# Kernel tuning notes

Hardware: AMD Instinct MI355X
Metric: run time of the kernel (lower is better)

The kernel has to match this reference:

```python
import jax, jax.numpy as jnp
import numpy as np

B, S, H = 1, 2048, 4096
NQ, NKV, D = 32, 8, 128
N_REP = NQ // NKV
SCALE = 1.0 / np.sqrt(D)
SOFTCAP = 30.0
EPS = 1e-5


def _rotate_half(x):
    x1, x2 = jnp.split(x, 2, axis=-1)
    return jnp.concatenate([-x2, x1], axis=-1)


def _rms_norm(x, w, eps=EPS):
    xf = x.astype(jnp.float32)
    norm = xf * jax.lax.rsqrt(jnp.mean(xf * xf, axis=-1, keepdims=True) + eps)
    return (w * norm).astype(x.dtype)


def setup_inputs() -> dict:
    key = jax.random.key(0)
    ks = jax.random.split(key, 8)
    hidden_states = jax.random.normal(ks[0], (B, S, H), dtype=jnp.float32)
    # causal additive mask
    causal = jnp.tril(jnp.ones((S, S), dtype=bool))
    attention_mask = jnp.where(causal, 0.0, -1e9)[None, None].astype(jnp.float32)
    # RoPE cache
    inv_freq = 1.0 / (10000.0 ** (np.arange(0, D, 2, dtype=np.float32) / D))
    t = np.arange(S, dtype=np.float32)
    freqs = np.outer(t, inv_freq)                      # (S, D/2)
    emb = np.concatenate([freqs, freqs], axis=-1)      # (S, D)
    cos = jnp.asarray(np.cos(emb))[None, None]         # (1,1,S,D)
    sin = jnp.asarray(np.sin(emb))[None, None]
    # params
    std = 0.02
    wq = jax.random.normal(ks[1], (NQ * D, H), dtype=jnp.float32) * std
    wk = jax.random.normal(ks[2], (NKV * D, H), dtype=jnp.float32) * std
    wv = jax.random.normal(ks[3], (NKV * D, H), dtype=jnp.float32) * std
    wo = jax.random.normal(ks[4], (H, NQ * D), dtype=jnp.float32) * std
    pre_norm_w = jnp.ones((H,), dtype=jnp.float32)
    q_norm_w = jnp.ones((D,), dtype=jnp.float32)
    k_norm_w = jnp.ones((D,), dtype=jnp.float32)
    return {
        "hidden_states": hidden_states, "attention_mask": attention_mask,
        "cos": cos, "sin": sin, "pre_norm_w": pre_norm_w,
        "wq": wq, "wk": wk, "wv": wv, "wo": wo,
        "q_norm_w": q_norm_w, "k_norm_w": k_norm_w,
    }


def reference(hidden_states, attention_mask, cos, sin, pre_norm_w,
              wq, wk, wv, wo, q_norm_w, k_norm_w):
    residual = hidden_states
    h = _rms_norm(hidden_states, pre_norm_w)
    bsz, seq_len, _ = h.shape
    # projections -> (b, heads, s, d)
    q = jnp.einsum('bsh,eh->bse', h, wq).reshape(bsz, seq_len, NQ, D).transpose(0, 2, 1, 3)
    k = jnp.einsum('bsh,eh->bse', h, wk).reshape(bsz, seq_len, NKV, D).transpose(0, 2, 1, 3)
    v = jnp.einsum('bsh,eh->bse', h, wv).reshape(bsz, seq_len, NKV, D).transpose(0, 2, 1, 3)
    # QK RMSNorm over head_dim
    q = _rms_norm(q, q_norm_w)
    k = _rms_norm(k, k_norm_w)
    # RoPE (full head_dim)
    q = q * cos + _rotate_half(q) * sin
    k = k * cos + _rotate_half(k) * sin
    # GQA: repeat kv heads
    k_exp = jnp.repeat(k, N_REP, axis=1)  # (b, NQ, s, d)
    v_exp = jnp.repeat(v, N_REP, axis=1)
    scores = jnp.einsum('bhqd,bhkd->bhqk', q, k_exp) * SCALE
    scores = SOFTCAP * jnp.tanh(scores / SOFTCAP)
    scores = scores + attention_mask
    probs = jax.nn.softmax(scores.astype(jnp.float32), axis=-1).astype(q.dtype)
    attn = jnp.einsum('bhqk,bhkd->bhqd', probs, v_exp)
    attn = attn.transpose(0, 2, 1, 3).reshape(bsz, seq_len, NQ * D)
    out = jnp.einsum('bse,he->bsh', attn, wo)
    return residual + out
```

## Files before the change

### kernel.cpp

```cpp
#include <hip/hip_runtime.h>
#include <cstdint>

typedef __bf16 bf16;
typedef __bf16 bf16x8 __attribute__((ext_vector_type(8)));
typedef __bf16 bf16x4 __attribute__((ext_vector_type(4)));
typedef float  f32x4  __attribute__((ext_vector_type(4)));

#define SEQ  2048
#define HID  4096
#define DH   128
#define NQH  32
#define NKVH 8
#define NTOT 6144
#define RSCALE 0.08838834764831845f
#define SOFTCAP 30.0f
#define L2E 1.4426950408889634f

__device__ __forceinline__ void gl2lds16(const void* g, void* l) {
  __builtin_amdgcn_global_load_lds(
      (const __attribute__((address_space(1))) unsigned int*)g,
      (__attribute__((address_space(3))) unsigned int*)l, 16, 0, 0);
}

__global__ void cvt_kernel(const float* __restrict__ in, bf16* __restrict__ out, int n4) {
  const int stride = gridDim.x * blockDim.x;
  for (int i = blockIdx.x * blockDim.x + threadIdx.x; i < n4; i += stride) {
    const float4 v = ((const float4*)in)[i];
    bf16x4 o = { (bf16)v.x, (bf16)v.y, (bf16)v.z, (bf16)v.w };
    *(bf16x4*)(out + (size_t)i * 4) = o;
  }
}

__global__ void rmsnorm_kernel(const float* __restrict__ x, const float* __restrict__ w,
                               bf16* __restrict__ out) {
  const int s = blockIdx.x;
  const float* xr = x + (size_t)s * HID;
  float4 v[4];
  float ss = 0.f;
#pragma unroll
  for (int j = 0; j < 4; ++j) {
    v[j] = ((const float4*)xr)[threadIdx.x + j * 256];
    ss += v[j].x * v[j].x + v[j].y * v[j].y + v[j].z * v[j].z + v[j].w * v[j].w;
  }
#pragma unroll
  for (int m = 1; m < 64; m <<= 1) ss += __shfl_xor(ss, m);
  __shared__ float red[4];
  if ((threadIdx.x & 63) == 0) red[threadIdx.x >> 6] = ss;
  __syncthreads();
  const float rn = rsqrtf((red[0] + red[1] + red[2] + red[3]) * (1.f / HID) + 1e-5f);
  bf16* orow = out + (size_t)s * HID;
#pragma unroll
  for (int j = 0; j < 4; ++j) {
    const int idx = (threadIdx.x + j * 256) * 4;
    const float4 wv = ((const float4*)w)[threadIdx.x + j * 256];
    bf16x4 o = { (bf16)(v[j].x * rn * wv.x), (bf16)(v[j].y * rn * wv.y),
                 (bf16)(v[j].z * rn * wv.z), (bf16)(v[j].w * rn * wv.w) };
    *(bf16x4*)(orow + idx) = o;
  }
}

template<bool FINAL>
__global__ __launch_bounds__(512, 2)
void gemm256(const bf16* __restrict__ A, const bf16* __restrict__ B,
             bf16* __restrict__ Cb, float* __restrict__ Cf,
             const float* __restrict__ resid, int M, int N, int K)
{
  extern __shared__ char smem[];
  const int tid  = threadIdx.x;
  const int lane = tid & 63;
  const int wave = tid >> 6;
  const int wm = wave >> 2, wn = wave & 3;

  const int gx = gridDim.x;
  const int nwg = gx * gridDim.y;
  int lin = blockIdx.x + gx * blockIdx.y;
  lin = (lin & 7) * (nwg >> 3) + (lin >> 3);
  const int m0 = (lin / gx) * 256;
  const int n0 = (lin % gx) * 256;

  auto Abuf = [&](int b) -> bf16* { return (bf16*)(smem + b * 65536); };
  auto Bbuf = [&](int b) -> bf16* { return (bf16*)(smem + b * 65536 + 32768); };

  auto stage = [&](int kt, int b) {
    bf16* Ad = Abuf(b);
    bf16* Bd = Bbuf(b);
#pragma unroll
    for (int i = 0; i < 4; ++i) {
      const int c = i * 8 + wave;
      const int row = c * 8 + (lane >> 3);
      const int col8 = (lane & 7) ^ (row & 7);
      gl2lds16(A + (size_t)(m0 + row) * K + kt + col8 * 8, Ad + c * 512);
    }
#pragma unroll
    for (int i = 0; i < 4; ++i) {
      const int c = i * 8 + wave;
      const int row = c * 8 + (lane >> 3);
      const int col8 = (lane & 7) ^ (row & 7);
      gl2lds16(B + (size_t)(n0 + row) * K + kt + col8 * 8, Bd + c * 512);
    }
  };

  f32x4 acc[8][4] = {};
  const int nt = K / 64;

  stage(0, 0);
  asm volatile("s_waitcnt vmcnt(0)" ::: "memory");
  __builtin_amdgcn_s_barrier();

  for (int t = 0; t < nt; ++t) {
    const int p = t & 1;
    const bf16* Ab = Abuf(p);
    const bf16* Bb = Bbuf(p);
    bf16x8 bfr[4][2];

#pragma unroll
    for (int q = 0; q < 4; ++q) {
      bf16x8 afr[2][2];
#pragma unroll
      for (int mi = 0; mi < 2; ++mi)
#pragma unroll
        for (int ks = 0; ks < 2; ++ks) {
          const int row = wm * 128 + q * 32 + mi * 16 + (lane & 15);
          const int slot = (ks * 4 + (lane >> 4)) ^ (row & 7);
          afr[mi][ks] = *(const bf16x8*)(Ab + row * 64 + slot * 8);
        }
      if (q == 0) {
#pragma unroll
        for (int ni = 0; ni < 4; ++ni)
#pragma unroll
          for (int ks = 0; ks < 2; ++ks) {
            const int row = wn * 64 + ni * 16 + (lane & 15);
            const int slot = (ks * 4 + (lane >> 4)) ^ (row & 7);
            bfr[ni][ks] = *(const bf16x8*)(Bb + row * 64 + slot * 8);
          }
        if (t + 1 < nt) stage((t + 1) * 64, p ^ 1);
      }

      __builtin_amdgcn_s_barrier();
      asm volatile("s_waitcnt lgkmcnt(0)" ::: "memory");
      __builtin_amdgcn_sched_barrier(0);
      __builtin_amdgcn_s_setprio(1);
#pragma unroll
      for (int ks = 0; ks < 2; ++ks)
#pragma unroll
        for (int mi = 0; mi < 2; ++mi)
#pragma unroll
          for (int ni = 0; ni < 4; ++ni)
            acc[q * 2 + mi][ni] = __builtin_amdgcn_mfma_f32_16x16x32_bf16(
                afr[mi][ks], bfr[ni][ks], acc[q * 2 + mi][ni], 0, 0, 0);
      __builtin_amdgcn_s_setprio(0);

      if (q == 3 && t + 1 < nt)
        asm volatile("s_waitcnt vmcnt(0)" ::: "memory");
      __builtin_amdgcn_s_barrier();
    }
  }

#pragma unroll
  for (int a = 0; a < 8; ++a) {
#pragma unroll
    for (int i = 0; i < 4; ++i) {
      const int m = m0 + wm * 128 + (a >> 1) * 32 + (a & 1) * 16 + (lane >> 4) * 4 + i;
#pragma unroll
      for (int ni = 0; ni < 4; ++ni) {
        const int n = n0 + wn * 64 + ni * 16 + (lane & 15);
        const float v = acc[a][ni][i];
        if constexpr (FINAL) {
          Cf[(size_t)m * N + n] = v + resid[(size_t)m * N + n];
        } else {
          Cb[(size_t)m * N + n] = (bf16)v;
        }
      }
    }
  }
}

__global__ void qkrope_kernel(const bf16* __restrict__ qkv,
                              const float* __restrict__ qw, const float* __restrict__ kw,
                              const float* __restrict__ cs, const float* __restrict__ sn,
                              bf16* __restrict__ qr, bf16* __restrict__ kr)
{
  const int w = blockIdx.x * 4 + (threadIdx.x >> 6);
  const int lane = threadIdx.x & 63;
  const int s = w / (NQH + NKVH);
  const int hh = w % (NQH + NKVH);
  const bf16* src; bf16* dst; const float* nw;
  if (hh < NQH) {
    src = qkv + (size_t)s * NTOT + hh * DH;
    dst = qr + ((size_t)hh * SEQ + s) * DH;
    nw = qw;
  } else {
    const int h2 = hh - NQH;
    src = qkv + (size_t)s * NTOT + 4096 + h2 * DH;
    dst = kr + ((size_t)h2 * SEQ + s) * DH;
    nw = kw;
  }
  const float x0 = (float)src[lane], x1 = (float)src[lane + 64];
  float ss = x0 * x0 + x1 * x1;
#pragma unroll
  for (int m = 1; m < 64; m <<= 1) ss += __shfl_xor(ss, m);
  const float rn = rsqrtf(ss * (1.f / DH) + 1e-5f);
  const float n0 = x0 * rn * nw[lane], n1 = x1 * rn * nw[lane + 64];
  const float c0 = cs[s * DH + lane],      s0 = sn[s * DH + lane];
  const float c1 = cs[s * DH + lane + 64], s1 = sn[s * DH + lane + 64];
  dst[lane]      = (bf16)(n0 * c0 - n1 * s0);
  dst[lane + 64] = (bf16)(n1 * c1 + n0 * s1);
}

__global__ void vtrans_kernel(const bf16* __restrict__ qkv, bf16* __restrict__ vt)
{
  __shared__ bf16 tbuf[64][33];
  const int s0 = blockIdx.x * 64;
  const int d0 = blockIdx.y * 32;
  const int h  = blockIdx.z;
  const int tid = threadIdx.x;
  {
    const int col = tid & 31, r0 = tid >> 5;
    for (int r = r0; r < 64; r += 8)
      tbuf[r][col] = qkv[(size_t)(s0 + r) * NTOT + 5120 + h * DH + d0 + col];
  }
  __syncthreads();
  {
    const int sc = tid & 63, dr0 = tid >> 6;
    for (int d = dr0; d < 32; d += 4)
      vt[((size_t)h * DH + d0 + d) * SEQ + s0 + sc] = tbuf[sc][d];
  }
}

__global__ __launch_bounds__(256, 2)
void attn_kernel(const bf16* __restrict__ Q, const bf16* __restrict__ Kr,
                 const bf16* __restrict__ Vt, bf16* __restrict__ Oa)
{
  __shared__ bf16 Ks[2][64 * 128];
  __shared__ bf16 Vs[2][128 * 64];
  __shared__ bf16 Ps[4][32 * 64];

  const int tid = threadIdx.x, lane = tid & 63, wave = tid >> 6;

  const int lin  = blockIdx.x + 16 * blockIdx.y;
  const int slot = lin >> 8, idx = lin & 255;
  const int bx   = slot ? (15 - (idx & 15)) : (idx & 15);
  const int head = (slot << 4) | (idx >> 4);
  const int kvh  = head >> 2;
  const int q0   = bx * 128;
  const int wq0  = q0 + wave * 32;

  const bf16* Qh = Q  + (size_t)head * SEQ * DH;
  const bf16* Kh = Kr + (size_t)kvh * SEQ * DH;
  const bf16* Vh = Vt + (size_t)kvh * DH * SEQ;

  bf16x8 qf[2][4];
#pragma unroll
  for (int mt = 0; mt < 2; ++mt)
#pragma unroll
    for (int kc = 0; kc < 4; ++kc) {
      const int r = wq0 + mt * 16 + (lane & 15);
      qf[mt][kc] = *(const bf16x8*)(Qh + (size_t)r * DH + kc * 32 + (lane >> 4) * 8);
    }

  float lsum[2][4] = {};
  f32x4 o_acc[2][8] = {};

  const int ntiles = q0 / 64 + 2;

  auto stage = [&](int t, int b) {
    const int kv0 = t * 64;
    bf16* Kd = &Ks[b][0];
    bf16* Vd = &Vs[b][0];
#pragma unroll
    for (int i2 = 0; i2 < 4; ++i2) {
      const int c = wave * 4 + i2;
      {
        const int row = c * 4 + (lane >> 4);
        const int col8 = (lane & 15) ^ (row & 15);
        gl2lds16(Kh + (size_t)(kv0 + row) * DH + col8 * 8, Kd + c * 512);
      }
      {
        const int row = c * 8 + (lane >> 3);
        const int col8 = (lane & 7) ^ (row & 7);
        gl2lds16(Vh + (size_t)row * SEQ + kv0 + col8 * 8, Vd + c * 512);
      }
    }
  };

  stage(0, 0);
  __syncthreads();

  const float ZS = RSCALE / SOFTCAP;
  const float A1 = RSCALE * L2E;
  const float B3 = -(ZS * ZS) * (1.f / 3.f);
  const float B5 = (2.f / 15.f) * (ZS * ZS) * (ZS * ZS);
  const float C  = SOFTCAP * L2E;

  for (int t = 0; t < ntiles; ++t) {
    const int cur = t & 1;
    if (t + 1 < ntiles) stage(t + 1, cur ^ 1);
    const int kv0 = t * 64;
    const bf16* Kb = &Ks[cur][0];
    const bf16* Vb = &Vs[cur][0];

    if (kv0 <= wq0 + 31) {
      f32x4 sc[2][4] = {};
      __builtin_amdgcn_s_setprio(1);
#pragma unroll
      for (int ks = 0; ks < 4; ++ks) {
        bf16x8 kf[4];
#pragma unroll
        for (int nt = 0; nt < 4; ++nt) {
          const int row = nt * 16 + (lane & 15);
          const int sl = (ks * 4 + (lane >> 4)) ^ (row & 15);
          kf[nt] = *(const bf16x8*)(Kb + row * 128 + sl * 8);
        }
#pragma unroll
        for (int mt = 0; mt < 2; ++mt)
#pragma unroll
          for (int nt = 0; nt < 4; ++nt)
            sc[mt][nt] = __builtin_amdgcn_mfma_f32_16x16x32_bf16(qf[mt][ks], kf[nt], sc[mt][nt], 0, 0, 0);
      }
      __builtin_amdgcn_s_setprio(0);

      if (kv0 + 63 <= wq0) {
#pragma unroll
        for (int mt = 0; mt < 2; ++mt)
#pragma unroll
          for (int i = 0; i < 4; ++i)
#pragma unroll
            for (int nt = 0; nt < 4; ++nt) {
              const float s = sc[mt][nt][i];
              const float w = s * s;
              const float poly = fmaf(fmaf(B5, w, B3), w, 1.f);
              const float p = __builtin_amdgcn_exp2f(fmaf(s * poly, A1, -C));
              sc[mt][nt][i] = p;
              lsum[mt][i] += p;
            }
      } else {
#pragma unroll
        for (int mt = 0; mt < 2; ++mt)
#pragma unroll
          for (int i = 0; i < 4; ++i) {
            const int qrow = wq0 + mt * 16 + (lane >> 4) * 4 + i;
#pragma unroll
            for (int nt = 0; nt < 4; ++nt) {
              const int col = kv0 + nt * 16 + (lane & 15);
              const float s = sc[mt][nt][i];
              const float w = s * s;
              const float poly = fmaf(fmaf(B5, w, B3), w, 1.f);
              float p = __builtin_amdgcn_exp2f(fmaf(s * poly, A1, -C));
              if (col > qrow) p = 0.f;
              sc[mt][nt][i] = p;
              lsum[mt][i] += p;
            }
          }
      }

#pragma unroll
      for (int mt = 0; mt < 2; ++mt)
#pragma unroll
        for (int nt = 0; nt < 4; ++nt)
#pragma unroll
          for (int i = 0; i < 4; ++i) {
            const int r = mt * 16 + (lane >> 4) * 4 + i;
            const int colb = nt * 16 + (lane & 15);
            const int sl = (colb >> 3) ^ (r & 7);
            Ps[wave][r * 64 + sl * 8 + (colb & 7)] = (bf16)sc[mt][nt][i];
          }
      asm volatile("s_waitcnt lgkmcnt(0)" ::: "memory");
      __builtin_amdgcn_sched_barrier(0);

      __builtin_amdgcn_s_setprio(1);
#pragma unroll
      for (int ks2 = 0; ks2 < 2; ++ks2) {
        bf16x8 pf[2];
#pragma unroll
        for (int mt = 0; mt < 2; ++mt) {
          const int r = mt * 16 + (lane & 15);
          const int sl = (ks2 * 4 + (lane >> 4)) ^ (r & 7);
          pf[mt] = *(const bf16x8*)(&Ps[wave][r * 64 + sl * 8]);
        }
#pragma unroll
        for (int nt = 0; nt < 8; ++nt) {
          const int row = nt * 16 + (lane & 15);
          const int sl = (ks2 * 4 + (lane >> 4)) ^ (row & 7);
          const bf16x8 vf = *(const bf16x8*)(Vb + row * 64 + sl * 8);
          o_acc[0][nt] = __builtin_amdgcn_mfma_f32_16x16x32_bf16(pf[0], vf, o_acc[0][nt], 0, 0, 0);
          o_acc[1][nt] = __builtin_amdgcn_mfma_f32_16x16x32_bf16(pf[1], vf, o_acc[1][nt], 0, 0, 0);
        }
      }
      __builtin_amdgcn_s_setprio(0);
    }
    __syncthreads();
  }

#pragma unroll
  for (int mt = 0; mt < 2; ++mt)
#pragma unroll
    for (int i = 0; i < 4; ++i) {
      float l = lsum[mt][i];
#pragma unroll
      for (int m = 1; m < 16; m <<= 1) l += __shfl_xor(l, m);
      const int qrow = wq0 + mt * 16 + (lane >> 4) * 4 + i;
      const float inv_l = 1.f / l;
#pragma unroll
      for (int nt = 0; nt < 8; ++nt) {
        const int d = nt * 16 + (lane & 15);
        Oa[(size_t)qrow * HID + head * DH + d] = (bf16)(o_acc[mt][nt][i] * inv_l);
      }
    }
}

extern "C" void kernel_launch(void* const* d_in, const int* in_sizes, int n_in,
                              void* d_out, int out_size, void* d_ws, size_t ws_size,
                              hipStream_t stream)
{
  const float* hidden = (const float*)d_in[0];
  const float* cosb   = (const float*)d_in[2];
  const float* sinb   = (const float*)d_in[3];
  const float* prew   = (const float*)d_in[4];
  const float* wq     = (const float*)d_in[5];
  const float* wk     = (const float*)d_in[6];
  const float* wv     = (const float*)d_in[7];
  const float* wo     = (const float*)d_in[8];
  const float* qnw    = (const float*)d_in[9];
  const float* knw    = (const float*)d_in[10];
  float* outp = (float*)d_out;
  char* ws = (char*)d_ws;

  bf16* wqkv = (bf16*)(ws + 0);
  bf16* hb   = (bf16*)(ws + 50331648);
  bf16* qkvp = (bf16*)(ws + 67108864);
  bf16* kr   = (bf16*)(ws + 92274688);
  bf16* vt   = (bf16*)(ws + 96468992);
  bf16* wob  = wqkv;

  cvt_kernel<<<2048, 256, 0, stream>>>(wq, wqkv, 4096 * HID / 4);
  cvt_kernel<<<1024, 256, 0, stream>>>(wk, wqkv + (size_t)4096 * HID, 1024 * HID / 4);
  cvt_kernel<<<1024, 256, 0, stream>>>(wv, wqkv + (size_t)5120 * HID, 1024 * HID / 4);
  rmsnorm_kernel<<<SEQ, 256, 0, stream>>>(hidden, prew, hb);

  gemm256<false><<<dim3(NTOT / 256, SEQ / 256), 512, 131072, stream>>>(
      hb, wqkv, qkvp, nullptr, nullptr, SEQ, NTOT, HID);

  cvt_kernel<<<2048, 256, 0, stream>>>(wo, wob, HID * HID / 4);

  qkrope_kernel<<<SEQ * (NQH + NKVH) / 4, 256, 0, stream>>>(qkvp, qnw, knw, cosb, sinb, hb, kr);
  vtrans_kernel<<<dim3(32, 4, 8), 256, 0, stream>>>(qkvp, vt);

  attn_kernel<<<dim3(16, 32), 256, 0, stream>>>(hb, kr, vt, qkvp);

  gemm256<true><<<dim3(HID / 256, SEQ / 256), 512, 131072, stream>>>(
      qkvp, wob, nullptr, outp, hidden, SEQ, HID, HID);
}
```

Measured before the change: 396.9 us.

## Replace GEMM with 5-slot ring pipeline and split-K atomic output projection

Replaces the double-buffered 64-wide K GEMM with a five-slot ring of 32-wide K chunks, keeping four stages of loads in flight, so global latency is hidden without running two workgroups per CU. The output projection is split into two K halves across grid z. Each half atomically adds into an output buffer that the RMSNorm kernel pre-fills with the residual. This raises parallelism for the 128-tile output GEMM, at the cost of float atomics, non-deterministic summation order, and 160KB of LDS limiting occupancy to one workgroup.

New measurement: 399.2 us. No clear change (+0.6%).

```diff
diff --git a/kernel.cpp b/kernel.cpp
--- a/kernel.cpp
+++ b/kernel.cpp
@@ -32,7 +32,7 @@
 }
 
 __global__ void rmsnorm_kernel(const float* __restrict__ x, const float* __restrict__ w,
-                               bf16* __restrict__ out) {
+                               bf16* __restrict__ out, float* __restrict__ res_out) {
   const int s = blockIdx.x;
   const float* xr = x + (size_t)s * HID;
   float4 v[4];
@@ -49,6 +49,7 @@
   __syncthreads();
   const float rn = rsqrtf((red[0] + red[1] + red[2] + red[3]) * (1.f / HID) + 1e-5f);
   bf16* orow = out + (size_t)s * HID;
+  float4* rrow = (float4*)(res_out + (size_t)s * HID);
 #pragma unroll
   for (int j = 0; j < 4; ++j) {
     const int idx = (threadIdx.x + j * 256) * 4;
@@ -56,14 +57,15 @@
     bf16x4 o = { (bf16)(v[j].x * rn * wv.x), (bf16)(v[j].y * rn * wv.y),
                  (bf16)(v[j].z * rn * wv.z), (bf16)(v[j].w * rn * wv.w) };
     *(bf16x4*)(orow + idx) = o;
+    rrow[threadIdx.x + j * 256] = v[j];
   }
 }
 
 template<bool FINAL>
-__global__ __launch_bounds__(512, 2)
-void gemm256(const bf16* __restrict__ A, const bf16* __restrict__ B,
-             bf16* __restrict__ Cb, float* __restrict__ Cf,
-             const float* __restrict__ resid, int M, int N, int K)
+__global__ __launch_bounds__(512, 1)
+void gemmring(const bf16* __restrict__ A, const bf16* __restrict__ B,
+              bf16* __restrict__ Cb, float* __restrict__ Cf,
+              int M, int N, int Ktot, int Klen)
 {
   extern __shared__ char smem[];
   const int tid  = threadIdx.x;
@@ -77,96 +79,76 @@
   lin = (lin & 7) * (nwg >> 3) + (lin >> 3);
   const int m0 = (lin / gx) * 256;
   const int n0 = (lin % gx) * 256;
-
-  auto Abuf = [&](int b) -> bf16* { return (bf16*)(smem + b * 65536); };
-  auto Bbuf = [&](int b) -> bf16* { return (bf16*)(smem + b * 65536 + 32768); };
-
-  auto stage = [&](int kt, int b) {
-    bf16* Ad = Abuf(b);
-    bf16* Bd = Bbuf(b);
+  const int k0 = blockIdx.z * Klen;
+
+  const int rsub = lane >> 2;
+  const int g8   = (((lane & 3) ^ (rsub & 3))) * 8;
+  auto stage = [&](int c, int sl) {
+    const int kt = k0 + c * 32;
+    char* base = smem + sl * 32768;
+#pragma unroll
+    for (int l = 0; l < 2; ++l) {
+      const int p = wave * 2 + l;
+      gl2lds16(A + (size_t)(m0 + p * 16 + rsub) * Ktot + kt + g8, base + p * 1024);
+    }
+#pragma unroll
+    for (int l = 0; l < 2; ++l) {
+      const int p = wave * 2 + l;
+      gl2lds16(B + (size_t)(n0 + p * 16 + rsub) * Ktot + kt + g8, base + 16384 + p * 1024);
+    }
+  };
+
+  f32x4 acc[8][4] = {};
+  const int n_ch = Klen / 32;
+
+  const int rl = lane & 15;
+  const int sw = ((lane >> 4) ^ (lane & 3)) * 8;
+
+  stage(0, 0); stage(1, 1); stage(2, 2); stage(3, 3);
+  asm volatile("s_waitcnt vmcnt(12)" ::: "memory");
+  asm volatile("s_barrier" ::: "memory");
+
+  int rs = 0, ss = 4;
+  for (int c = 0; c < n_ch; ++c) {
+    if (c + 4 < n_ch) stage(c + 4, ss);
+    const bf16* Ab = (const bf16*)(smem + rs * 32768);
+    const bf16* Bb = (const bf16*)(smem + rs * 32768 + 16384);
+    bf16x8 afr[8], bfr[4];
+#pragma unroll
+    for (int mi = 0; mi < 8; ++mi)
+      afr[mi] = *(const bf16x8*)(Ab + (wm * 128 + mi * 16 + rl) * 32 + sw);
+#pragma unroll
+    for (int ni = 0; ni < 4; ++ni)
+      bfr[ni] = *(const bf16x8*)(Bb + (wn * 64 + ni * 16 + rl) * 32 + sw);
+    asm volatile("s_waitcnt lgkmcnt(0)" ::: "memory");
+    __builtin_amdgcn_sched_barrier(0);
+    __builtin_amdgcn_s_setprio(1);
+#pragma unroll
+    for (int mi = 0; mi < 8; ++mi)
+#pragma unroll
+      for (int ni = 0; ni < 4; ++ni)
+        acc[mi][ni] = __builtin_amdgcn_mfma_f32_16x16x32_bf16(afr[mi], bfr[ni], acc[mi][ni], 0, 0, 0);
+    __builtin_amdgcn_s_setprio(0);
+    if (c + 5 <= n_ch)      { asm volatile("s_waitcnt vmcnt(12)" ::: "memory"); }
+    else if (c + 4 == n_ch) { asm volatile("s_waitcnt vmcnt(8)"  ::: "memory"); }
+    else if (c + 3 == n_ch) { asm volatile("s_waitcnt vmcnt(4)"  ::: "memory"); }
+    else if (c + 2 == n_ch) { asm volatile("s_waitcnt vmcnt(0)"  ::: "memory"); }
+    asm volatile("s_barrier" ::: "memory");
+    rs = (rs == 4) ? 0 : rs + 1;
+    ss = (ss == 4) ? 0 : ss + 1;
+  }
+
+#pragma unroll
+  for (int mi = 0; mi < 8; ++mi) {
 #pragma unroll
     for (int i = 0; i < 4; ++i) {
-      const int c = i * 8 + wave;
-      const int row = c * 8 + (lane >> 3);
-      const int col8 = (lane & 7) ^ (row & 7);
-      gl2lds16(A + (size_t)(m0 + row) * K + kt + col8 * 8, Ad + c * 512);
-    }
-#pragma unroll
-    for (int i = 0; i < 4; ++i) {
-      const int c = i * 8 + wave;
-      const int row = c * 8 + (lane >> 3);
-      const int col8 = (lane & 7) ^ (row & 7);
-      gl2lds16(B + (size_t)(n0 + row) * K + kt + col8 * 8, Bd + c * 512);
-    }
-  };
-
-  f32x4 acc[8][4] = {};
-  const int nt = K / 64;
-
-  stage(0, 0);
-  asm volatile("s_waitcnt vmcnt(0)" ::: "memory");
-  __builtin_amdgcn_s_barrier();
-
-  for (int t = 0; t < nt; ++t) {
-    const int p = t & 1;
-    const bf16* Ab = Abuf(p);
-    const bf16* Bb = Bbuf(p);
-    bf16x8 bfr[4][2];
-
-#pragma unroll
-    for (int q = 0; q < 4; ++q) {
-      bf16x8 afr[2][2];
-#pragma unroll
-      for (int mi = 0; mi < 2; ++mi)
-#pragma unroll
-        for (int ks = 0; ks < 2; ++ks) {
-          const int row = wm * 128 + q * 32 + mi * 16 + (lane & 15);
-          const int slot = (ks * 4 + (lane >> 4)) ^ (row & 7);
-          afr[mi][ks] = *(const bf16x8*)(Ab + row * 64 + slot * 8);
-        }
-      if (q == 0) {
-#pragma unroll
-        for (int ni = 0; ni < 4; ++ni)
-#pragma unroll
-          for (int ks = 0; ks < 2; ++ks) {
-            const int row = wn * 64 + ni * 16 + (lane & 15);
-            const int slot = (ks * 4 + (lane >> 4)) ^ (row & 7);
-            bfr[ni][ks] = *(const bf16x8*)(Bb + row * 64 + slot * 8);
-          }
-        if (t + 1 < nt) stage((t + 1) * 64, p ^ 1);
-      }
-
-      __builtin_amdgcn_s_barrier();
-      asm volatile("s_waitcnt lgkmcnt(0)" ::: "memory");
-      __builtin_amdgcn_sched_barrier(0);
-      __builtin_amdgcn_s_setprio(1);
-#pragma unroll
-      for (int ks = 0; ks < 2; ++ks)
-#pragma unroll
-        for (int mi = 0; mi < 2; ++mi)
-#pragma unroll
-          for (int ni = 0; ni < 4; ++ni)
-            acc[q * 2 + mi][ni] = __builtin_amdgcn_mfma_f32_16x16x32_bf16(
-                afr[mi][ks], bfr[ni][ks], acc[q * 2 + mi][ni], 0, 0, 0);
-      __builtin_amdgcn_s_setprio(0);
-
-      if (q == 3 && t + 1 < nt)
-        asm volatile("s_waitcnt vmcnt(0)" ::: "memory");
-      __builtin_amdgcn_s_barrier();
-    }
-  }
-
-#pragma unroll
-  for (int a = 0; a < 8; ++a) {
-#pragma unroll
-    for (int i = 0; i < 4; ++i) {
-      const int m = m0 + wm * 128 + (a >> 1) * 32 + (a & 1) * 16 + (lane >> 4) * 4 + i;
+      const int m = m0 + wm * 128 + mi * 16 + (lane >> 4) * 4 + i;
 #pragma unroll
       for (int ni = 0; ni < 4; ++ni) {
         const int n = n0 + wn * 64 + ni * 16 + (lane & 15);
-        const float v = acc[a][ni][i];
+        const float v = acc[mi][ni][i];
         if constexpr (FINAL) {
-          Cf[(size_t)m * N + n] = v + resid[(size_t)m * N + n];
+          atomicAdd(Cf + (size_t)m * N + n, v);
         } else {
           Cb[(size_t)m * N + n] = (bf16)v;
         }
@@ -435,10 +417,10 @@
   cvt_kernel<<<2048, 256, 0, stream>>>(wq, wqkv, 4096 * HID / 4);
   cvt_kernel<<<1024, 256, 0, stream>>>(wk, wqkv + (size_t)4096 * HID, 1024 * HID / 4);
   cvt_kernel<<<1024, 256, 0, stream>>>(wv, wqkv + (size_t)5120 * HID, 1024 * HID / 4);
-  rmsnorm_kernel<<<SEQ, 256, 0, stream>>>(hidden, prew, hb);
-
-  gemm256<false><<<dim3(NTOT / 256, SEQ / 256), 512, 131072, stream>>>(
-      hb, wqkv, qkvp, nullptr, nullptr, SEQ, NTOT, HID);
+  rmsnorm_kernel<<<SEQ, 256, 0, stream>>>(hidden, prew, hb, outp);
+
+  gemmring<false><<<dim3(NTOT / 256, SEQ / 256, 1), 512, 163840, stream>>>(
+      hb, wqkv, qkvp, nullptr, SEQ, NTOT, HID, HID);
 
   cvt_kernel<<<2048, 256, 0, stream>>>(wo, wob, HID * HID / 4);
 
@@ -447,6 +429,6 @@
 
   attn_kernel<<<dim3(16, 32), 256, 0, stream>>>(hb, kr, vt, qkvp);
 
-  gemm256<true><<<dim3(HID / 256, SEQ / 256), 512, 131072, stream>>>(
-      qkvp, wob, nullptr, outp, hidden, SEQ, HID, HID);
-}
+  gemmring<true><<<dim3(HID / 256, SEQ / 256, 2), 512, 163840, stream>>>(
+      qkvp, wob, nullptr, outp, SEQ, HID, HID, HID / 2);
+}
```
